# Performance work log

Measured on AMD Instinct MI355X. Metric: run time of the kernel, lower is better.

## Reference

```python
import jax, jax.numpy as jnp
import numpy as np

N = 50000   # nodes
E = 600000  # edges
D = 128     # in/out features


def setup_inputs() -> dict:
    key = jax.random.key(0)
    k1, k2, k3, k4, k5, k6 = jax.random.split(key, 6)
    input = jax.random.normal(k1, (N, D), dtype=jnp.float32)
    W = jax.random.normal(k2, (D, D), dtype=jnp.float32) * (1.0 / np.sqrt(D))
    b = jax.random.normal(k3, (D,), dtype=jnp.float32) * 0.01
    adj_row = jnp.sort(jax.random.randint(k4, (E,), 0, N, dtype=jnp.int32))
    adj_col = jax.random.randint(k5, (E,), 0, N, dtype=jnp.int32)
    adj_val = jax.random.uniform(k6, (E,), dtype=jnp.float32)
    return {"input": input, "W": W, "b": b,
            "adj_row": adj_row, "adj_col": adj_col, "adj_val": adj_val}


def reference(input, W, b, adj_row, adj_col, adj_val):
    # support = Linear(input)  -> [N, D]
    support = jnp.einsum('nd,od->no', input, W) + b
    # sparse adj (COO) @ support : gather source rows, scale by edge value,
    # scatter-add into destination rows.
    msgs = support[adj_col] * adj_val[:, None]           # [E, D]
    agg = jax.ops.segment_sum(msgs, adj_row, num_segments=input.shape[0])
    return jnp.tanh(agg)
```

## Files before the change

### kernel.cpp

```cpp
#include <hip/hip_runtime.h>
#include <hip/hip_fp16.h>
#include <cmath>

#define DF 128
#define WPITCHH 136

typedef _Float16 f16x8 __attribute__((ext_vector_type(8)));
typedef float    f32x4 __attribute__((ext_vector_type(4)));

__global__ __launch_bounds__(256)
void gemm_mfma_kernel(const float* __restrict__ X, const _Float16* __restrict__ Wh,
                      const float* __restrict__ bias, __half* __restrict__ S,
                      int N)
{
    __shared__ _Float16 Wl[DF * WPITCHH];

    const int t    = threadIdx.x;
    const int lane = t & 63;
    const int l15  = lane & 15;
    const int q    = lane >> 4;
    const int m0   = (blockIdx.x * 4 + (t >> 6)) * 16;

    #pragma unroll
    for (int l = 0; l < 8; ++l) {
        int flat = l * 256 + t;
        int r    = flat >> 4;
        int c8   = (flat & 15) * 8;
        f16x8 v = *(const f16x8*)(Wh + (size_t)r * DF + c8);
        *(f16x8*)(Wl + r * WPITCHH + c8) = v;
    }
    __syncthreads();
    if (m0 >= N) return;

    f32x4 acc[8];
    #pragma unroll
    for (int nt = 0; nt < 8; ++nt) acc[nt] = (f32x4){0.f, 0.f, 0.f, 0.f};

    const int arow = min(m0 + l15, N - 1);
    #pragma unroll
    for (int kc = 0; kc < DF; kc += 32) {
        const float* xp = X + (size_t)arow * DF + kc + q * 8;
        float4 xa = *(const float4*)xp;
        float4 xb = *(const float4*)(xp + 4);
        f16x8 A;
        A[0] = (_Float16)xa.x; A[1] = (_Float16)xa.y;
        A[2] = (_Float16)xa.z; A[3] = (_Float16)xa.w;
        A[4] = (_Float16)xb.x; A[5] = (_Float16)xb.y;
        A[6] = (_Float16)xb.z; A[7] = (_Float16)xb.w;
        #pragma unroll
        for (int nt = 0; nt < 8; ++nt) {
            f16x8 B = *(const f16x8*)(Wl + (nt * 16 + l15) * WPITCHH + kc + q * 8);
            acc[nt] = __builtin_amdgcn_mfma_f32_16x16x32_f16(A, B, acc[nt], 0, 0, 0);
        }
    }

    #pragma unroll
    for (int nt = 0; nt < 8; ++nt) {
        float bj = bias[nt * 16 + l15];
        #pragma unroll
        for (int r = 0; r < 4; ++r) {
            int gr = m0 + q * 4 + r;
            if (gr < N)
                S[(size_t)gr * DF + nt * 16 + l15] = __float2half(acc[nt][r] + bj);
        }
    }
}

__global__ __launch_bounds__(256)
void build_meta_kernel(const int* __restrict__ arow, const int* __restrict__ acol,
                       const float* __restrict__ aval, const float* __restrict__ W,
                       int* __restrict__ rowptr, int2* __restrict__ pk,
                       _Float16* __restrict__ Wh, int N, int E)
{
    int e = blockIdx.x * 256 + threadIdx.x;
    if (e >= E) return;
    if (e < DF * DF) Wh[e] = (_Float16)W[e];
    pk[e] = make_int2(acol[e] << 8, __float_as_int(aval[e]));
    int r = arow[e];
    int rprev = (e == 0) ? -1 : arow[e - 1];
    for (int n = rprev + 1; n <= r; ++n) rowptr[n] = e;
    if (e == E - 1) {
        for (int n = r + 1; n <= N; ++n) rowptr[n] = E;
    }
}

__global__ __launch_bounds__(256)
void agg_tanh_kernel(const __half* __restrict__ S, const int* __restrict__ rowptr,
                     const int2* __restrict__ pk, float* __restrict__ out, int Nn)
{
    const int n = __builtin_amdgcn_readfirstlane(blockIdx.x * 4 + (threadIdx.x >> 6));
    if (n >= Nn) return;
    const int lane = threadIdx.x & 63;
    const int g    = lane >> 4;
    const int fb   = (lane & 15) * 16;

    const int start = rowptr[n];
    const int end   = rowptr[n + 1];
    const char* Sb  = (const char*)S;

    float acc[8];
    #pragma unroll
    for (int i = 0; i < 8; ++i) acc[i] = 0.f;

    for (int base = start; base < end; base += 8) {
        const int e0 = base + g;
        const int e1 = base + 4 + g;
        int2 p0 = (e0 < end) ? pk[e0] : make_int2(0, 0);
        int2 p1 = (e1 < end) ? pk[e1] : make_int2(0, 0);
        f16x8 h0 = *(const f16x8*)(Sb + (size_t)(unsigned)p0.x + fb);
        f16x8 h1 = *(const f16x8*)(Sb + (size_t)(unsigned)p1.x + fb);
        const float v0 = __int_as_float(p0.y);
        const float v1 = __int_as_float(p1.y);
        #pragma unroll
        for (int i = 0; i < 8; ++i)
            acc[i] += (float)h0[i] * v0 + (float)h1[i] * v1;
    }

    #pragma unroll
    for (int i = 0; i < 8; ++i) {
        acc[i] += __shfl_xor(acc[i], 16);
        acc[i] += __shfl_xor(acc[i], 32);
    }

    if (g == 0) {
        float4 o0, o1;
        o0.x = tanhf(acc[0]); o0.y = tanhf(acc[1]);
        o0.z = tanhf(acc[2]); o0.w = tanhf(acc[3]);
        o1.x = tanhf(acc[4]); o1.y = tanhf(acc[5]);
        o1.z = tanhf(acc[6]); o1.w = tanhf(acc[7]);
        float* op = out + (size_t)n * DF + (lane & 15) * 8;
        *(float4*)op       = o0;
        *(float4*)(op + 4) = o1;
    }
}

extern "C" void kernel_launch(void* const* d_in, const int* in_sizes, int n_in,
                              void* d_out, int out_size, void* d_ws, size_t ws_size,
                              hipStream_t stream)
{
    const float* X    = (const float*)d_in[0];
    const float* W    = (const float*)d_in[1];
    const float* bias = (const float*)d_in[2];
    const int*   arow = (const int*)  d_in[3];
    const int*   acol = (const int*)  d_in[4];
    const float* aval = (const float*)d_in[5];
    float* out = (float*)d_out;

    const int N = in_sizes[0] / DF;
    const int E = in_sizes[3];

    __half*   S      = (__half*)d_ws;
    _Float16* Wh     = (_Float16*)((char*)d_ws + (size_t)N * DF * sizeof(__half));
    int*      rowptr = (int*)((char*)Wh + (size_t)DF * DF * sizeof(_Float16));
    int2*     pk     = (int2*)(rowptr + (N + 2));

    build_meta_kernel<<<(E + 255) / 256, 256, 0, stream>>>(arow, acol, aval, W,
                                                           rowptr, pk, Wh, N, E);

    gemm_mfma_kernel<<<(N + 63) / 64, 256, 0, stream>>>(X, Wh, bias, S, N);

    agg_tanh_kernel<<<(N + 3) / 4, 256, 0, stream>>>(S, rowptr, pk, out, N);
}
```

Baseline: 129.0 us.

## Map one node per 16 lanes in aggregation and vectorize GEMM output stores

The aggregation kernel now assigns 16 lanes per node instead of a full 64-lane wavefront, so each wave handles four nodes. Each 16-lane group walks its node's edges four at a time, which removes the cross-group shuffle reduction. The GEMM swaps the MFMA operands so each lane holds a row-contiguous output, allowing vectorized 4-wide half stores and vector bias loads instead of scalar stores. The trade-off is divergence: nodes in one wave with different degrees leave lanes idle, and edge loads per lane become less parallel.

```diff
diff --git a/kernel.cpp b/kernel.cpp
--- a/kernel.cpp
+++ b/kernel.cpp
@@ -6,6 +6,7 @@
 #define WPITCHH 136
 
 typedef _Float16 f16x8 __attribute__((ext_vector_type(8)));
+typedef _Float16 f16x4 __attribute__((ext_vector_type(4)));
 typedef float    f32x4 __attribute__((ext_vector_type(4)));
 
 __global__ __launch_bounds__(256)
@@ -36,10 +37,10 @@
     #pragma unroll
     for (int nt = 0; nt < 8; ++nt) acc[nt] = (f32x4){0.f, 0.f, 0.f, 0.f};
 
-    const int arow = min(m0 + l15, N - 1);
+    const int xrow = min(m0 + l15, N - 1);
     #pragma unroll
     for (int kc = 0; kc < DF; kc += 32) {
-        const float* xp = X + (size_t)arow * DF + kc + q * 8;
+        const float* xp = X + (size_t)xrow * DF + kc + q * 8;
         float4 xa = *(const float4*)xp;
         float4 xb = *(const float4*)(xp + 4);
         f16x8 A;
@@ -50,18 +51,22 @@
         #pragma unroll
         for (int nt = 0; nt < 8; ++nt) {
             f16x8 B = *(const f16x8*)(Wl + (nt * 16 + l15) * WPITCHH + kc + q * 8);
-            acc[nt] = __builtin_amdgcn_mfma_f32_16x16x32_f16(A, B, acc[nt], 0, 0, 0);
+            acc[nt] = __builtin_amdgcn_mfma_f32_16x16x32_f16(B, A, acc[nt], 0, 0, 0);
         }
     }
 
-    #pragma unroll
-    for (int nt = 0; nt < 8; ++nt) {
-        float bj = bias[nt * 16 + l15];
+    const int mrow = m0 + l15;
+    if (mrow < N) {
+        _Float16* rowp = (_Float16*)S + (size_t)mrow * DF;
         #pragma unroll
-        for (int r = 0; r < 4; ++r) {
-            int gr = m0 + q * 4 + r;
-            if (gr < N)
-                S[(size_t)gr * DF + nt * 16 + l15] = __float2half(acc[nt][r] + bj);
+        for (int nt = 0; nt < 8; ++nt) {
+            float4 bv = *(const float4*)(bias + nt * 16 + q * 4);
+            f16x4 hv;
+            hv[0] = (_Float16)(acc[nt][0] + bv.x);
+            hv[1] = (_Float16)(acc[nt][1] + bv.y);
+            hv[2] = (_Float16)(acc[nt][2] + bv.z);
+            hv[3] = (_Float16)(acc[nt][3] + bv.w);
+            *(f16x4*)(rowp + nt * 16 + q * 4) = hv;
         }
     }
 }
@@ -88,11 +93,10 @@
 void agg_tanh_kernel(const __half* __restrict__ S, const int* __restrict__ rowptr,
                      const int2* __restrict__ pk, float* __restrict__ out, int Nn)
 {
-    const int n = __builtin_amdgcn_readfirstlane(blockIdx.x * 4 + (threadIdx.x >> 6));
+    const int n  = (blockIdx.x * 256 + threadIdx.x) >> 4;
     if (n >= Nn) return;
-    const int lane = threadIdx.x & 63;
-    const int g    = lane >> 4;
-    const int fb   = (lane & 15) * 16;
+    const int f  = threadIdx.x & 15;
+    const int fb = f * 16;
 
     const int start = rowptr[n];
     const int end   = rowptr[n + 1];
@@ -102,36 +106,34 @@
     #pragma unroll
     for (int i = 0; i < 8; ++i) acc[i] = 0.f;
 
-    for (int base = start; base < end; base += 8) {
-        const int e0 = base + g;
-        const int e1 = base + 4 + g;
-        int2 p0 = (e0 < end) ? pk[e0] : make_int2(0, 0);
-        int2 p1 = (e1 < end) ? pk[e1] : make_int2(0, 0);
+    for (int e = start; e < end; e += 4) {
+        int2 p0 = pk[e];
+        int2 p1 = (e + 1 < end) ? pk[e + 1] : make_int2(0, 0);
+        int2 p2 = (e + 2 < end) ? pk[e + 2] : make_int2(0, 0);
+        int2 p3 = (e + 3 < end) ? pk[e + 3] : make_int2(0, 0);
         f16x8 h0 = *(const f16x8*)(Sb + (size_t)(unsigned)p0.x + fb);
         f16x8 h1 = *(const f16x8*)(Sb + (size_t)(unsigned)p1.x + fb);
+        f16x8 h2 = *(const f16x8*)(Sb + (size_t)(unsigned)p2.x + fb);
+        f16x8 h3 = *(const f16x8*)(Sb + (size_t)(unsigned)p3.x + fb);
         const float v0 = __int_as_float(p0.y);
         const float v1 = __int_as_float(p1.y);
+        const float v2 = __int_as_float(p2.y);
+        const float v3 = __int_as_float(p3.y);
         #pragma unroll
-        for (int i = 0; i < 8; ++i)
-            acc[i] += (float)h0[i] * v0 + (float)h1[i] * v1;
+        for (int i = 0; i < 8; ++i) {
+            acc[i] += (float)h0[i] * v0 + (float)h1[i] * v1
+                    + (float)h2[i] * v2 + (float)h3[i] * v3;
+        }
     }
 
-    #pragma unroll
-    for (int i = 0; i < 8; ++i) {
-        acc[i] += __shfl_xor(acc[i], 16);
-        acc[i] += __shfl_xor(acc[i], 32);
-    }
-
-    if (g == 0) {
-        float4 o0, o1;
-        o0.x = tanhf(acc[0]); o0.y = tanhf(acc[1]);
-        o0.z = tanhf(acc[2]); o0.w = tanhf(acc[3]);
-        o1.x = tanhf(acc[4]); o1.y = tanhf(acc[5]);
-        o1.z = tanhf(acc[6]); o1.w = tanhf(acc[7]);
-        float* op = out + (size_t)n * DF + (lane & 15) * 8;
-        *(float4*)op       = o0;
-        *(float4*)(op + 4) = o1;
-    }
+    float4 o0, o1;
+    o0.x = tanhf(acc[0]); o0.y = tanhf(acc[1]);
+    o0.z = tanhf(acc[2]); o0.w = tanhf(acc[3]);
+    o1.x = tanhf(acc[4]); o1.y = tanhf(acc[5]);
+    o1.z = tanhf(acc[6]); o1.w = tanhf(acc[7]);
+    float* op = out + (size_t)n * DF + f * 8;
+    *(float4*)op       = o0;
+    *(float4*)(op + 4) = o1;
 }
 
 extern "C" void kernel_launch(void* const* d_in, const int* in_sizes, int n_in,
@@ -159,5 +161,5 @@
 
     gemm_mfma_kernel<<<(N + 63) / 64, 256, 0, stream>>>(X, Wh, bias, S, N);
 
-    agg_tanh_kernel<<<(N + 3) / 4, 256, 0, stream>>>(S, rowptr, pk, out, N);
+    agg_tanh_kernel<<<(N * 16 + 255) / 256, 256, 0, stream>>>(S, rowptr, pk, out, N);
 }
```

After: 124.1 us. 1.04x faster.
